# Kernel optimization log

Hardware: AMD Instinct MI355X
Metric: run time of the kernel (lower is better)

Reference implementation:

```python
import jax, jax.numpy as jnp
import numpy as np

D_MODEL = 1024
N_HEADS = 16
D_FF = 4096
B, T = 4, 2048
EPS = 1e-5


def layernorm(x, g, b):
    mu = jnp.mean(x, axis=-1, keepdims=True)
    var = jnp.var(x, axis=-1, keepdims=True)
    return (x - mu) * jax.lax.rsqrt(var + EPS) * g + b


def setup_inputs() -> dict:
    key = jax.random.key(0)
    ks = jax.random.split(key, 8)
    s = 0.02
    return {
        "x": jax.random.normal(ks[0], (B, T, D_MODEL), jnp.float32),
        "ln1_g": jnp.ones((D_MODEL,), jnp.float32),
        "ln1_b": jnp.zeros((D_MODEL,), jnp.float32),
        "wq": jax.random.normal(ks[1], (D_MODEL, D_MODEL), jnp.float32) * s,
        "bq": jnp.zeros((D_MODEL,), jnp.float32),
        "wk": jax.random.normal(ks[2], (D_MODEL, D_MODEL), jnp.float32) * s,
        "bk": jnp.zeros((D_MODEL,), jnp.float32),
        "wv": jax.random.normal(ks[3], (D_MODEL, D_MODEL), jnp.float32) * s,
        "bv": jnp.zeros((D_MODEL,), jnp.float32),
        "wo": jax.random.normal(ks[4], (D_MODEL, D_MODEL), jnp.float32) * s,
        "bo": jnp.zeros((D_MODEL,), jnp.float32),
        "ln2_g": jnp.ones((D_MODEL,), jnp.float32),
        "ln2_b": jnp.zeros((D_MODEL,), jnp.float32),
        "w1": jax.random.normal(ks[5], (D_FF, D_MODEL), jnp.float32) * s,
        "b1": jnp.zeros((D_FF,), jnp.float32),
        "w2": jax.random.normal(ks[6], (D_MODEL, D_FF), jnp.float32) * s,
        "b2": jnp.zeros((D_MODEL,), jnp.float32),
    }


def reference(x, ln1_g, ln1_b, wq, bq, wk, bk, wv, bv, wo, bo,
              ln2_g, ln2_b, w1, b1, w2, b2):
    d_k = D_MODEL // N_HEADS
    # --- attention sublayer (pre-LN) ---
    h = layernorm(x, ln1_g, ln1_b)                       # [B,T,D]
    q = (h @ wq.T + bq).reshape(B, T, N_HEADS, d_k)
    k = (h @ wk.T + bk).reshape(B, T, N_HEADS, d_k)
    v = (h @ wv.T + bv).reshape(B, T, N_HEADS, d_k)
    scores = jnp.einsum("bqhd,bkhd->bhqk", q, k) / jnp.sqrt(jnp.float32(d_k))
    attn = jax.nn.softmax(scores, axis=-1)               # [B,H,T,T]
    o = jnp.einsum("bhqk,bkhd->bqhd", attn, v).reshape(B, T, D_MODEL)
    x = x + (o @ wo.T + bo)
    # --- FFN sublayer ---
    h2 = layernorm(x, ln2_g, ln2_b)
    h2 = jax.nn.gelu(h2 @ w1.T + b1, approximate=False)  # torch GELU = exact erf
    x = x + (h2 @ w2.T + b2)
    return x
```

## Files before the change

kernel.cpp:

```cpp
#include <hip/hip_runtime.h>
#include <math.h>


#define D_MODEL 1024
#define D_FF    4096
#define NH      16
#define BATCH   4
#define SEQ     2048
#define DK      64
#define MTOK    (BATCH*SEQ)
#define NBH     (BATCH*NH)

typedef __bf16 bf16;
typedef _Float16 f16;
typedef bf16  bf16x4 __attribute__((ext_vector_type(4)));
typedef bf16  bf16x8 __attribute__((ext_vector_type(8)));
typedef f16   f16x4  __attribute__((ext_vector_type(4)));
typedef __fp16 hf16x2 __attribute__((ext_vector_type(2)));
typedef __fp16 hf16x4 __attribute__((ext_vector_type(4)));
typedef float f32x4  __attribute__((ext_vector_type(4)));

__device__ __forceinline__ void gload_lds16(const void* g, void* l) {
  __builtin_amdgcn_global_load_lds(
      (__attribute__((address_space(1))) void*)g,
      (__attribute__((address_space(3))) void*)l, 16, 0, 0);
}

#define BAR() __builtin_amdgcn_s_barrier()
#define WAIT_VM0() do { asm volatile("s_waitcnt vmcnt(0)" ::: "memory"); \
  __builtin_amdgcn_sched_barrier(0); } while (0)
#define WAIT_LGKM0() do { asm volatile("s_waitcnt lgkmcnt(0)" ::: "memory"); } while (0)

__global__ __launch_bounds__(256) void cast_w(const float* __restrict__ s,
                                              bf16* __restrict__ d, int n) {
  int i = (blockIdx.x * 256 + threadIdx.x) * 4;
  if (i >= n) return;
  float4 v = *(const float4*)(s + i);
  bf16x4 o;
  o[0] = (bf16)v.x; o[1] = (bf16)v.y; o[2] = (bf16)v.z; o[3] = (bf16)v.w;
  *(bf16x4*)(d + i) = o;
}

__global__ __launch_bounds__(256) void ln_kernel(const float* __restrict__ x,
                                                 const float* __restrict__ g,
                                                 const float* __restrict__ b,
                                                 bf16* __restrict__ out) {
  int row = blockIdx.x;
  int tid = threadIdx.x;
  const float* xr = x + (size_t)row * D_MODEL;
  float4 v = *(const float4*)(xr + tid * 4);
  float s  = v.x + v.y + v.z + v.w;
  float sq = v.x*v.x + v.y*v.y + v.z*v.z + v.w*v.w;
  #pragma unroll
  for (int off = 1; off < 64; off <<= 1) {
    s  += __shfl_xor(s,  off, 64);
    sq += __shfl_xor(sq, off, 64);
  }
  __shared__ float ls[4], lq[4];
  int wid = tid >> 6, lane = tid & 63;
  if (lane == 0) { ls[wid] = s; lq[wid] = sq; }
  __syncthreads();
  s  = ls[0] + ls[1] + ls[2] + ls[3];
  sq = lq[0] + lq[1] + lq[2] + lq[3];
  float mu   = s * (1.0f / D_MODEL);
  float var  = sq * (1.0f / D_MODEL) - mu * mu;
  float rstd = rsqrtf(var + 1e-5f);
  float4 gv = *(const float4*)(g + tid * 4);
  float4 bv = *(const float4*)(b + tid * 4);
  bf16x4 o;
  o[0] = (bf16)((v.x - mu) * rstd * gv.x + bv.x);
  o[1] = (bf16)((v.y - mu) * rstd * gv.y + bv.y);
  o[2] = (bf16)((v.z - mu) * rstd * gv.z + bv.z);
  o[3] = (bf16)((v.w - mu) * rstd * gv.w + bv.w);
  *(bf16x4*)(out + (size_t)row * D_MODEL + tid * 4) = o;
}

enum { EP_QKV = 0, EP_RESID = 1, EP_GELU = 2 };

#define QSCALE 0.18033688011112042f

template <int EP, int CFG>
__global__ __launch_bounds__(512) void gemm8p(
    const bf16* __restrict__ A, const bf16* __restrict__ W,
    const float* __restrict__ bias,
    const float* __restrict__ resid,
    float* __restrict__ out_f32,
    bf16* __restrict__ out_bf,
    int M, int N, int K) {
  constexpr int BM  = CFG ? 128 : 256;
  constexpr int BK  = CFG ? 64 : 32;
  constexpr int WM  = CFG ? 64 : 128;
  constexpr int FRN = WM / 16;
  constexpr int FRP = FRN / 2;
  constexpr int KKN = BK / 32;
  constexpr int RB  = BK * 2;
  constexpr int GR  = RB / 16;
  constexpr int RSH = CFG ? 7 : 6;
  constexpr int AB  = 16384;
  constexpr int TB  = AB + 256 * BK * 2;
  constexpr int L   = TB / 8192;
  constexpr int Lh  = L / 2;

  __shared__ char lds[3 * TB];

  int tiles_n = N >> 8;
  int nwg = (M / BM) * tiles_n;
  int bid = blockIdx.x;
  int swz = (bid & 7) * (nwg >> 3) + (bid >> 3);
  int bm = swz / tiles_n, bn = swz % tiles_n;
  int m0 = bm * BM, n0 = bn << 8;
  int tid = threadIdx.x, wid = tid >> 6, lane = tid & 63;
  int wm = wid >> 2, wn = wid & 3;
  int l15 = lane & 15, l4 = lane >> 4;

  f32x4 acc[FRN][4];
  #pragma unroll
  for (int i = 0; i < FRN; i++)
    #pragma unroll
    for (int j = 0; j < 4; j++)
      #pragma unroll
      for (int e = 0; e < 4; e++) acc[i][j][e] = 0.f;

  auto STAGE = [&](int kt, int nb, int part) {
    char* buf = lds + nb * TB;
    #pragma unroll
    for (int l = part * Lh; l < part * Lh + Lh; ++l) {
      bool isA = l < 2;
      int o = (isA ? l : l - 2) * 8192 + tid * 16;
      int row = o >> RSH;
      int g = (o >> 4) & (GR - 1);
      int gs = g ^ (CFG ? (row & 7) : ((row >> 1) & 3));
      const bf16* src = (isA ? A + (size_t)(m0 + row) * K
                             : W + (size_t)(n0 + row) * K) + kt * BK + gs * 8;
      gload_lds16(src, buf + (isA ? 0 : AB) + o);
    }
  };

  int nt = K / BK;
  STAGE(0, 0, 0); STAGE(0, 0, 1);
  STAGE(1, 1, 0); STAGE(1, 1, 1);
  if constexpr (CFG) { asm volatile("s_waitcnt vmcnt(6)" ::: "memory"); }
  else               { asm volatile("s_waitcnt vmcnt(4)" ::: "memory"); }
  __builtin_amdgcn_sched_barrier(0);
  BAR();

  bf16x8 bfr[4][KKN];
  for (int t = 0; t < nt; ++t) {
    int cb = t % 3, nb = cb >= 1 ? cb - 1 : 2;
    bool ds_ = (t + 2) < nt;
    const char* bc = lds + cb * TB;

    bf16x8 af[FRP][KKN];
    #pragma unroll
    for (int f = 0; f < FRP; ++f)
      #pragma unroll
      for (int kk = 0; kk < KKN; ++kk) {
        int row = wm * WM + f * 16 + l15;
        int g = (kk * 4 + l4) ^ (CFG ? (row & 7) : ((row >> 1) & 3));
        af[f][kk] = *(const bf16x8*)(bc + row * RB + g * 16);
      }
    #pragma unroll
    for (int fc = 0; fc < 4; ++fc)
      #pragma unroll
      for (int kk = 0; kk < KKN; ++kk) {
        int row = wn * 64 + fc * 16 + l15;
        int g = (kk * 4 + l4) ^ (CFG ? (row & 7) : ((row >> 1) & 3));
        bfr[fc][kk] = *(const bf16x8*)(bc + AB + row * RB + g * 16);
      }
    if (ds_) STAGE(t + 2, nb, 0);
    BAR();
    WAIT_LGKM0();
    __builtin_amdgcn_s_setprio(1);
    #pragma unroll
    for (int f = 0; f < FRP; ++f)
      #pragma unroll
      for (int fc = 0; fc < 4; ++fc)
        #pragma unroll
        for (int kk = 0; kk < KKN; ++kk)
          acc[f][fc] = __builtin_amdgcn_mfma_f32_16x16x32_bf16(af[f][kk], bfr[fc][kk],
                                                               acc[f][fc], 0, 0, 0);
    __builtin_amdgcn_s_setprio(0);
    BAR();

    bf16x8 af1[FRP][KKN];
    #pragma unroll
    for (int f = 0; f < FRP; ++f)
      #pragma unroll
      for (int kk = 0; kk < KKN; ++kk) {
        int row = wm * WM + (FRP + f) * 16 + l15;
        int g = (kk * 4 + l4) ^ (CFG ? (row & 7) : ((row >> 1) & 3));
        af1[f][kk] = *(const bf16x8*)(bc + row * RB + g * 16);
      }
    if (ds_) STAGE(t + 2, nb, 1);
    BAR();
    WAIT_LGKM0();
    __builtin_amdgcn_s_setprio(1);
    #pragma unroll
    for (int f = 0; f < FRP; ++f)
      #pragma unroll
      for (int fc = 0; fc < 4; ++fc)
        #pragma unroll
        for (int kk = 0; kk < KKN; ++kk)
          acc[FRP + f][fc] = __builtin_amdgcn_mfma_f32_16x16x32_bf16(af1[f][kk], bfr[fc][kk],
                                                                     acc[FRP + f][fc], 0, 0, 0);
    __builtin_amdgcn_s_setprio(0);
    if (t < nt - 2) {
      if constexpr (CFG) { asm volatile("s_waitcnt vmcnt(6)" ::: "memory"); }
      else               { asm volatile("s_waitcnt vmcnt(4)" ::: "memory"); }
      __builtin_amdgcn_sched_barrier(0);
    } else if (t == nt - 2) {
      WAIT_VM0();
    }
    BAR();
  }

  if (EP == EP_QKV) {
    #pragma unroll
    for (int i = 0; i < FRN; i++)
      #pragma unroll
      for (int j = 0; j < 4; j++) {
        int gm0 = m0 + wm * WM + i * 16 + (l4 << 2);
        int gn  = n0 + wn * 64 + j * 16 + l15;
        int which = gn >> 10;
        int nn = gn & 1023, head = nn >> 6, d = nn & 63;
        int bb = gm0 >> 11, t = gm0 & 2047;
        float bv = bias[gn];
        if (which == 2) {
          f16x4 pk;
          #pragma unroll
          for (int jj = 0; jj < 4; jj++) pk[jj] = (f16)(acc[i][j][jj] + bv);
          *(f16x4*)((f16*)out_bf + (size_t)2 * NBH * SEQ * DK +
                    ((size_t)(bb * NH + head) * DK + d) * SEQ + t) = pk;
        } else {
          float scale = (which == 0) ? QSCALE : 1.0f;
          #pragma unroll
          for (int jj = 0; jj < 4; jj++) {
            float cv = (acc[i][j][jj] + bv) * scale;
            size_t idx = (size_t)which * (NBH * SEQ * DK) +
                         ((size_t)(bb * NH + head) * SEQ + (t + jj)) * DK + d;
            out_bf[idx] = (bf16)cv;
          }
        }
      }
  } else {
    #pragma unroll
    for (int i = 0; i < FRN; i++)
      #pragma unroll
      for (int j = 0; j < 4; j++)
        #pragma unroll
        for (int jj = 0; jj < 4; jj++) {
          int gm = m0 + wm * WM + i * 16 + (l4 << 2) + jj;
          int gn = n0 + wn * 64 + j * 16 + l15;
          float cv = acc[i][j][jj] + bias[gn];
          if (EP == EP_RESID) {
            size_t idx = (size_t)gm * N + gn;
            out_f32[idx] = resid[idx] + cv;
          } else {
            float ge = 0.5f * cv * (1.0f + erff(cv * 0.70710678118654752f));
            out_bf[(size_t)gm * N + gn] = (bf16)ge;
          }
        }
  }
}

__global__ __launch_bounds__(256) void attn_kernel(
    const bf16* __restrict__ q, const bf16* __restrict__ k,
    const f16* __restrict__ vt, bf16* __restrict__ o) {
  __shared__ bf16 kt_lds[2][128 * 64];
  __shared__ f16  vt_lds[2][64 * 128];
  int bid = blockIdx.x;
  int bh = bid >> 5;
  int qt = bid & 31;
  int t0 = qt << 6;
  int tid = threadIdx.x, wid = tid >> 6, lane = tid & 63;
  int l15 = lane & 15, l4 = lane >> 4;

  int kb0 = l15 * 128 + ((l4 ^ (l15 & 7)) << 4);
  int kb1 = l15 * 128 + (((4 + l4) ^ (l15 & 7)) << 4);
  int vb[8];
  #pragma unroll
  for (int kk = 0; kk < 8; kk++)
    vb[kk] = l15 * 256 + (((((kk << 1) + (l4 >> 1)) ^ l15) << 4) + ((l4 & 1) << 3));

  const bf16* qbase = q + ((size_t)bh * SEQ + t0 + wid * 16 + l15) * DK;
  bf16x8 qf[2];
  qf[0] = *(const bf16x8*)(qbase + (l4 << 3));
  qf[1] = *(const bf16x8*)(qbase + 32 + (l4 << 3));

  const f16x4 vones = {(f16)1.f, (f16)1.f, (f16)1.f, (f16)1.f};
  float m_run = -1e30f;
  f32x4 acc_o[4];
  f32x4 acc_l;
  #pragma unroll
  for (int nd = 0; nd < 4; nd++)
    #pragma unroll
    for (int e = 0; e < 4; e++) acc_o[nd][e] = 0.f;
  #pragma unroll
  for (int e = 0; e < 4; e++) acc_l[e] = 0.f;

  int rK = tid >> 3;
  int cK = ((tid & 7) ^ (rK & 7)) << 3;
  const bf16* gK = k + ((size_t)bh * SEQ + rK) * DK + cK;
  int rV = tid >> 4;
  int cV = ((tid & 15) ^ rV) << 3;
  const f16* gV = vt + ((size_t)bh * DK + rV) * SEQ + cV;

  auto stage = [&](int buf, int t) {
    const bf16* gKt = gK + ((size_t)t * 128) * DK;
    const f16*  gVt = gV + t * 128;
    char* dK = (char*)&kt_lds[buf][0] + (wid << 10);
    char* dV = (char*)&vt_lds[buf][0] + (wid << 10);
    #pragma unroll
    for (int it = 0; it < 4; ++it) {
      gload_lds16(gKt + (size_t)(it * 32) * DK, dK + it * 4096);
      gload_lds16(gVt + (size_t)(it * 16) * SEQ, dV + it * 4096);
    }
  };

  stage(0, 0);
  WAIT_VM0();
  BAR();

  for (int t = 0; t < SEQ / 128; ++t) {
    int cur = t & 1;
    if (t < SEQ / 128 - 1) stage(cur ^ 1, t + 1);
    const char* kbase = (const char*)&kt_lds[cur][0];
    const char* vbase = (const char*)&vt_lds[cur][0];

    f32x4 accs[8];
    #pragma unroll
    for (int n = 0; n < 8; n++)
      #pragma unroll
      for (int e = 0; e < 4; e++) accs[n][e] = 0.f;
    __builtin_amdgcn_s_setprio(1);
    #pragma unroll
    for (int n = 0; n < 8; n++) {
      bf16x8 kf0 = *(const bf16x8*)(kbase + kb0 + n * 2048);
      bf16x8 kf1 = *(const bf16x8*)(kbase + kb1 + n * 2048);
      accs[n] = __builtin_amdgcn_mfma_f32_16x16x32_bf16(kf0, qf[0], accs[n], 0, 0, 0);
      accs[n] = __builtin_amdgcn_mfma_f32_16x16x32_bf16(kf1, qf[1], accs[n], 0, 0, 0);
    }
    __builtin_amdgcn_s_setprio(0);

    float mloc = -1e30f;
    #pragma unroll
    for (int n = 0; n < 8; n++) {
      float a0 = fmaxf(accs[n][0], accs[n][1]);
      float a1 = fmaxf(accs[n][2], accs[n][3]);
      mloc = fmaxf(mloc, fmaxf(a0, a1));
    }
    float mt = fmaxf(mloc, __shfl_xor(mloc, 16, 64));
    mt = fmaxf(mt, __shfl_xor(mt, 32, 64));
    if (__any(mt > m_run + 8.0f)) {
      float mn = fmaxf(m_run, mt);
      float sc = __builtin_amdgcn_exp2f(m_run - mn);
      m_run = mn;
      float scr0 = __shfl(sc, l4 * 20 + 0, 64);
      float scr1 = __shfl(sc, l4 * 20 + 1, 64);
      float scr2 = __shfl(sc, l4 * 20 + 2, 64);
      float scr3 = __shfl(sc, l4 * 20 + 3, 64);
      #pragma unroll
      for (int nd = 0; nd < 4; nd++) {
        acc_o[nd][0] *= scr0; acc_o[nd][1] *= scr1;
        acc_o[nd][2] *= scr2; acc_o[nd][3] *= scr3;
      }
      acc_l[0] *= scr0; acc_l[1] *= scr1; acc_l[2] *= scr2; acc_l[3] *= scr3;
    }
    f16x4 pa[8];
    #pragma unroll
    for (int n = 0; n < 8; n++) {
      float e0 = __builtin_amdgcn_exp2f(accs[n][0] - m_run);
      float e1 = __builtin_amdgcn_exp2f(accs[n][1] - m_run);
      float e2 = __builtin_amdgcn_exp2f(accs[n][2] - m_run);
      float e3 = __builtin_amdgcn_exp2f(accs[n][3] - m_run);
      hf16x2 lo = __builtin_amdgcn_cvt_pkrtz(e0, e1);
      hf16x2 hi = __builtin_amdgcn_cvt_pkrtz(e2, e3);
      hf16x4 cmb = __builtin_shufflevector(lo, hi, 0, 1, 2, 3);
      pa[n] = __builtin_bit_cast(f16x4, cmb);
    }

    __builtin_amdgcn_s_setprio(1);
    #pragma unroll
    for (int kk = 0; kk < 8; kk++) {
      #pragma unroll
      for (int nd = 0; nd < 4; nd++) {
        f16x4 vf = *(const f16x4*)(vbase + vb[kk] + nd * 4096);
        acc_o[nd] = __builtin_amdgcn_mfma_f32_16x16x16f16(pa[kk], vf, acc_o[nd], 0, 0, 0);
      }
      acc_l = __builtin_amdgcn_mfma_f32_16x16x16f16(pa[kk], vones, acc_l, 0, 0, 0);
    }
    __builtin_amdgcn_s_setprio(0);

    if (t < SEQ / 128 - 1) { WAIT_VM0(); }
    BAR();
  }

  float rl0 = 1.0f / acc_l[0], rl1 = 1.0f / acc_l[1];
  float rl2 = 1.0f / acc_l[2], rl3 = 1.0f / acc_l[3];
  int bb = bh >> 4, hh = bh & 15;
  #pragma unroll
  for (int nd = 0; nd < 4; nd++) {
    int d = nd * 16 + l15;
    int rowb = t0 + wid * 16 + l4 * 4;
    o[((size_t)bb * SEQ + rowb + 0) * D_MODEL + hh * DK + d] = (bf16)(acc_o[nd][0] * rl0);
    o[((size_t)bb * SEQ + rowb + 1) * D_MODEL + hh * DK + d] = (bf16)(acc_o[nd][1] * rl1);
    o[((size_t)bb * SEQ + rowb + 2) * D_MODEL + hh * DK + d] = (bf16)(acc_o[nd][2] * rl2);
    o[((size_t)bb * SEQ + rowb + 3) * D_MODEL + hh * DK + d] = (bf16)(acc_o[nd][3] * rl3);
  }
}

extern "C" void kernel_launch(void* const* d_in, const int* in_sizes, int n_in,
                              void* d_out, int out_size, void* d_ws, size_t ws_size,
                              hipStream_t stream) {
  const float* x    = (const float*)d_in[0];
  const float* ln1g = (const float*)d_in[1];
  const float* ln1b = (const float*)d_in[2];
  const float* wq   = (const float*)d_in[3];
  const float* bq   = (const float*)d_in[4];
  const float* wk   = (const float*)d_in[5];
  const float* bk   = (const float*)d_in[6];
  const float* wv   = (const float*)d_in[7];
  const float* bv   = (const float*)d_in[8];
  const float* wo   = (const float*)d_in[9];
  const float* bo   = (const float*)d_in[10];
  const float* ln2g = (const float*)d_in[11];
  const float* ln2b = (const float*)d_in[12];
  const float* w1   = (const float*)d_in[13];
  const float* b1   = (const float*)d_in[14];
  const float* w2   = (const float*)d_in[15];
  const float* b2   = (const float*)d_in[16];
  float* out = (float*)d_out;

  char* ws = (char*)d_ws;
  bf16* wqkv_b = (bf16*)(ws);
  bf16* wo_b   = (bf16*)(ws + ((size_t)6  << 20));
  bf16* w1_b   = (bf16*)(ws + ((size_t)8  << 20));
  bf16* w2_b   = (bf16*)(ws + ((size_t)16 << 20));
  bf16* h_b    = (bf16*)(ws + ((size_t)24 << 20));
  bf16* qkv_b  = (bf16*)(ws + ((size_t)40 << 20));
  bf16* o_b    = (bf16*)(ws + ((size_t)88 << 20));
  bf16* ffn1_b = (bf16*)(ws + ((size_t)40 << 20));
  float* bqkv  = (float*)(ws + ((size_t)104 << 20));

  cast_w<<<1024, 256, 0, stream>>>(wq, wqkv_b, 1 << 20);
  cast_w<<<1024, 256, 0, stream>>>(wk, wqkv_b + (1 << 20), 1 << 20);
  cast_w<<<1024, 256, 0, stream>>>(wv, wqkv_b + (2 << 20), 1 << 20);
  cast_w<<<1024, 256, 0, stream>>>(wo, wo_b, 1 << 20);
  cast_w<<<4096, 256, 0, stream>>>(w1, w1_b, 1 << 22);
  cast_w<<<4096, 256, 0, stream>>>(w2, w2_b, 1 << 22);
  (void)hipMemcpyAsync(bqkv,        bq, 4096, hipMemcpyDeviceToDevice, stream);
  (void)hipMemcpyAsync(bqkv + 1024, bk, 4096, hipMemcpyDeviceToDevice, stream);
  (void)hipMemcpyAsync(bqkv + 2048, bv, 4096, hipMemcpyDeviceToDevice, stream);

  ln_kernel<<<MTOK, 256, 0, stream>>>(x, ln1g, ln1b, h_b);
  gemm8p<EP_QKV, 1><<<768, 512, 0, stream>>>(h_b, wqkv_b, bqkv, nullptr, nullptr,
                                             qkv_b, MTOK, 3072, 1024);
  attn_kernel<<<NBH * 32, 256, 0, stream>>>(qkv_b, qkv_b + (size_t)NBH * SEQ * DK,
                                            (const f16*)(qkv_b + (size_t)2 * NBH * SEQ * DK),
                                            o_b);
  gemm8p<EP_RESID, 1><<<256, 512, 0, stream>>>(o_b, wo_b, bo, x, out, nullptr,
                                               MTOK, 1024, 1024);
  ln_kernel<<<MTOK, 256, 0, stream>>>(out, ln2g, ln2b, h_b);
  gemm8p<EP_GELU, 0><<<512, 512, 0, stream>>>(h_b, w1_b, b1, nullptr, nullptr,
                                              ffn1_b, MTOK, 4096, 1024);
  gemm8p<EP_RESID, 1><<<256, 512, 0, stream>>>(ffn1_b, w2_b, b2, out, out, nullptr,
                                               MTOK, 1024, 4096);
}
```

Measured before the change: 476.7 us.

## Split-K the FFN2 GEMM with fp16 partials, retile QKV, relayout attention V LDS

The FFN2 GEMM is split into two K halves. Each half runs as a 256-row-tile block and writes fp16 partial sums, and a new combine kernel adds the residual, the bias and both partials. The QKV projection switches to the larger 256-row tile config with fewer blocks. The attention kernel's V tile in LDS is reorganised into two 64-key halves with a new XOR swizzle and new staging addresses, presumably to cut LDS bank conflicts. The trade-offs are extra global traffic for the partials plus an extra launch, and lower precision because the partials are stored as fp16.

```diff
diff --git a/kernel.cpp b/kernel.cpp
--- a/kernel.cpp
+++ b/kernel.cpp
@@ -75,7 +75,25 @@
   *(bf16x4*)(out + (size_t)row * D_MODEL + tid * 4) = o;
 }
 
-enum { EP_QKV = 0, EP_RESID = 1, EP_GELU = 2 };
+__global__ __launch_bounds__(256) void ffn2_combine(const float* __restrict__ x,
+                                                    const float* __restrict__ b2,
+                                                    const f16* __restrict__ p0,
+                                                    const f16* __restrict__ p1,
+                                                    float* __restrict__ out) {
+  size_t i = ((size_t)blockIdx.x * 256 + threadIdx.x) * 4;
+  float4 xv = *(const float4*)(x + i);
+  f16x4 a = *(const f16x4*)(p0 + i);
+  f16x4 c = *(const f16x4*)(p1 + i);
+  float4 bv = *(const float4*)(b2 + (i & 1023));
+  float4 o;
+  o.x = xv.x + bv.x + (float)a[0] + (float)c[0];
+  o.y = xv.y + bv.y + (float)a[1] + (float)c[1];
+  o.z = xv.z + bv.z + (float)a[2] + (float)c[2];
+  o.w = xv.w + bv.w + (float)a[3] + (float)c[3];
+  *(float4*)(out + i) = o;
+}
+
+enum { EP_QKV = 0, EP_RESID = 1, EP_GELU = 2, EP_PART = 3 };
 
 #define QSCALE 0.18033688011112042f
 
@@ -86,7 +104,7 @@
     const float* __restrict__ resid,
     float* __restrict__ out_f32,
     bf16* __restrict__ out_bf,
-    int M, int N, int K) {
+    int M, int N, int K, int lda) {
   constexpr int BM  = CFG ? 128 : 256;
   constexpr int BK  = CFG ? 64 : 32;
   constexpr int WM  = CFG ? 64 : 128;
@@ -106,6 +124,8 @@
   int tiles_n = N >> 8;
   int nwg = (M / BM) * tiles_n;
   int bid = blockIdx.x;
+  int kh = 0;
+  if (EP == EP_PART) { if (bid >= nwg) { kh = 1; bid -= nwg; } }
   int swz = (bid & 7) * (nwg >> 3) + (bid >> 3);
   int bm = swz / tiles_n, bn = swz % tiles_n;
   int m0 = bm * BM, n0 = bn << 8;
@@ -113,6 +133,9 @@
   int wm = wid >> 2, wn = wid & 3;
   int l15 = lane & 15, l4 = lane >> 4;
 
+  const bf16* Ap = A + (size_t)kh * K;
+  const bf16* Wp = W + (size_t)kh * K;
+
   f32x4 acc[FRN][4];
   #pragma unroll
   for (int i = 0; i < FRN; i++)
@@ -130,8 +153,8 @@
       int row = o >> RSH;
       int g = (o >> 4) & (GR - 1);
       int gs = g ^ (CFG ? (row & 7) : ((row >> 1) & 3));
-      const bf16* src = (isA ? A + (size_t)(m0 + row) * K
-                             : W + (size_t)(n0 + row) * K) + kt * BK + gs * 8;
+      const bf16* src = (isA ? Ap + (size_t)(m0 + row) * lda
+                             : Wp + (size_t)(n0 + row) * lda) + kt * BK + gs * 8;
       gload_lds16(src, buf + (isA ? 0 : AB) + o);
     }
   };
@@ -242,6 +265,18 @@
           }
         }
       }
+  } else if (EP == EP_PART) {
+    f16* dst = kh ? (f16*)out_bf : (f16*)out_f32;
+    #pragma unroll
+    for (int i = 0; i < FRN; i++)
+      #pragma unroll
+      for (int j = 0; j < 4; j++)
+        #pragma unroll
+        for (int jj = 0; jj < 4; jj++) {
+          int gm = m0 + wm * WM + i * 16 + (l4 << 2) + jj;
+          int gn = n0 + wn * 64 + j * 16 + l15;
+          dst[(size_t)gm * N + gn] = (f16)acc[i][j][jj];
+        }
   } else {
     #pragma unroll
     for (int i = 0; i < FRN; i++)
@@ -267,7 +302,7 @@
     const bf16* __restrict__ q, const bf16* __restrict__ k,
     const f16* __restrict__ vt, bf16* __restrict__ o) {
   __shared__ bf16 kt_lds[2][128 * 64];
-  __shared__ f16  vt_lds[2][64 * 128];
+  __shared__ f16  vt_lds[2][128 * 64];
   int bid = blockIdx.x;
   int bh = bid >> 5;
   int qt = bid & 31;
@@ -280,7 +315,8 @@
   int vb[8];
   #pragma unroll
   for (int kk = 0; kk < 8; kk++)
-    vb[kk] = l15 * 256 + (((((kk << 1) + (l4 >> 1)) ^ l15) << 4) + ((l4 & 1) << 3));
+    vb[kk] = ((kk >> 2) << 13) + l15 * 128 +
+             (((((kk & 3) << 1) + (l4 >> 1)) ^ (l15 & 7)) << 4) + ((l4 & 1) << 3);
 
   const bf16* qbase = q + ((size_t)bh * SEQ + t0 + wid * 16 + l15) * DK;
   bf16x8 qf[2];
@@ -301,19 +337,24 @@
   int rK = tid >> 3;
   int cK = ((tid & 7) ^ (rK & 7)) << 3;
   const bf16* gK = k + ((size_t)bh * SEQ + rK) * DK + cK;
-  int rV = tid >> 4;
-  int cV = ((tid & 15) ^ rV) << 3;
-  const f16* gV = vt + ((size_t)bh * DK + rV) * SEQ + cV;
+  const f16* gVsrc[4];
+  #pragma unroll
+  for (int it = 0; it < 4; ++it) {
+    int R = it * 32 + wid * 8 + (lane >> 3);
+    int g = lane & 7;
+    gVsrc[it] = vt + (size_t)bh * DK * SEQ + (size_t)(R & 63) * SEQ +
+                ((R >> 6) << 6) + ((g ^ (R & 7)) << 3);
+  }
 
   auto stage = [&](int buf, int t) {
     const bf16* gKt = gK + ((size_t)t * 128) * DK;
-    const f16*  gVt = gV + t * 128;
+    int kv0 = t * 128;
     char* dK = (char*)&kt_lds[buf][0] + (wid << 10);
     char* dV = (char*)&vt_lds[buf][0] + (wid << 10);
     #pragma unroll
     for (int it = 0; it < 4; ++it) {
       gload_lds16(gKt + (size_t)(it * 32) * DK, dK + it * 4096);
-      gload_lds16(gVt + (size_t)(it * 16) * SEQ, dV + it * 4096);
+      gload_lds16(gVsrc[it] + kv0, dV + it * 4096);
     }
   };
 
@@ -384,7 +425,7 @@
     for (int kk = 0; kk < 8; kk++) {
       #pragma unroll
       for (int nd = 0; nd < 4; nd++) {
-        f16x4 vf = *(const f16x4*)(vbase + vb[kk] + nd * 4096);
+        f16x4 vf = *(const f16x4*)(vbase + vb[kk] + nd * 2048);
         acc_o[nd] = __builtin_amdgcn_mfma_f32_16x16x16f16(pa[kk], vf, acc_o[nd], 0, 0, 0);
       }
       acc_l = __builtin_amdgcn_mfma_f32_16x16x16f16(pa[kk], vones, acc_l, 0, 0, 0);
@@ -441,6 +482,8 @@
   bf16* o_b    = (bf16*)(ws + ((size_t)88 << 20));
   bf16* ffn1_b = (bf16*)(ws + ((size_t)40 << 20));
   float* bqkv  = (float*)(ws + ((size_t)104 << 20));
+  f16* p0      = (f16*)(ws);
+  f16* p1      = (f16*)(ws + ((size_t)24 << 20));
 
   cast_w<<<1024, 256, 0, stream>>>(wq, wqkv_b, 1 << 20);
   cast_w<<<1024, 256, 0, stream>>>(wk, wqkv_b + (1 << 20), 1 << 20);
@@ -453,16 +496,18 @@
   (void)hipMemcpyAsync(bqkv + 2048, bv, 4096, hipMemcpyDeviceToDevice, stream);
 
   ln_kernel<<<MTOK, 256, 0, stream>>>(x, ln1g, ln1b, h_b);
-  gemm8p<EP_QKV, 1><<<768, 512, 0, stream>>>(h_b, wqkv_b, bqkv, nullptr, nullptr,
-                                             qkv_b, MTOK, 3072, 1024);
+  gemm8p<EP_QKV, 0><<<384, 512, 0, stream>>>(h_b, wqkv_b, bqkv, nullptr, nullptr,
+                                             qkv_b, MTOK, 3072, 1024, 1024);
   attn_kernel<<<NBH * 32, 256, 0, stream>>>(qkv_b, qkv_b + (size_t)NBH * SEQ * DK,
                                             (const f16*)(qkv_b + (size_t)2 * NBH * SEQ * DK),
                                             o_b);
   gemm8p<EP_RESID, 1><<<256, 512, 0, stream>>>(o_b, wo_b, bo, x, out, nullptr,
-                                               MTOK, 1024, 1024);
+                                               MTOK, 1024, 1024, 1024);
   ln_kernel<<<MTOK, 256, 0, stream>>>(out, ln2g, ln2b, h_b);
   gemm8p<EP_GELU, 0><<<512, 512, 0, stream>>>(h_b, w1_b, b1, nullptr, nullptr,
-                                              ffn1_b, MTOK, 4096, 1024);
-  gemm8p<EP_RESID, 1><<<256, 512, 0, stream>>>(ffn1_b, w2_b, b2, out, out, nullptr,
-                                               MTOK, 1024, 4096);
-}
+                                              ffn1_b, MTOK, 4096, 1024, 1024);
+  gemm8p<EP_PART, 0><<<256, 512, 0, stream>>>(ffn1_b, w2_b, nullptr, nullptr,
+                                              (float*)p0, (bf16*)p1,
+                                              MTOK, 1024, 2048, 4096);
+  ffn2_combine<<<8192, 256, 0, stream>>>(out, b2, p0, p1, out);
+}
```

After: 485.9 us. About the same (+1.9%).

## Use 16x16x32 f16 MFMA for attention PV with permuted V layout

Applied to the files above, without the earlier changes.

Switches the attention P·V product from 16x16x16 f16 MFMAs to the wider 16x16x32 f16 MFMA, packing eight softmax probabilities per operand. To make this work, the QKV epilogue writes V-transposed with a permuted sequence order, and the LDS staging addresses and swizzle for V are reworked so each lane reads 8 contiguous f16 values with one 16-byte LDS load. The goal is half as many MFMA issues and LDS reads in the PV loop, at the cost of a tightly coupled permutation between the QKV writer and the attention reader that must stay consistent.

```diff
diff --git a/kernel.cpp b/kernel.cpp
--- a/kernel.cpp
+++ b/kernel.cpp
@@ -16,8 +16,10 @@
 typedef bf16  bf16x4 __attribute__((ext_vector_type(4)));
 typedef bf16  bf16x8 __attribute__((ext_vector_type(8)));
 typedef f16   f16x4  __attribute__((ext_vector_type(4)));
+typedef f16   f16x8  __attribute__((ext_vector_type(8)));
 typedef __fp16 hf16x2 __attribute__((ext_vector_type(2)));
 typedef __fp16 hf16x4 __attribute__((ext_vector_type(4)));
+typedef __fp16 hf16x8 __attribute__((ext_vector_type(8)));
 typedef float f32x4  __attribute__((ext_vector_type(4)));
 
 __device__ __forceinline__ void gload_lds16(const void* g, void* l) {
@@ -226,11 +228,12 @@
         int bb = gm0 >> 11, t = gm0 & 2047;
         float bv = bias[gn];
         if (which == 2) {
+          int sbase = (t & ~31) + ((t >> 2) & 3) * 8 + ((t >> 4) & 1) * 4;
           f16x4 pk;
           #pragma unroll
           for (int jj = 0; jj < 4; jj++) pk[jj] = (f16)(acc[i][j][jj] + bv);
           *(f16x4*)((f16*)out_bf + (size_t)2 * NBH * SEQ * DK +
-                    ((size_t)(bb * NH + head) * DK + d) * SEQ + t) = pk;
+                    ((size_t)(bb * NH + head) * DK + d) * SEQ + sbase) = pk;
         } else {
           float scale = (which == 0) ? QSCALE : 1.0f;
           #pragma unroll
@@ -277,17 +280,19 @@
 
   int kb0 = l15 * 128 + ((l4 ^ (l15 & 7)) << 4);
   int kb1 = l15 * 128 + (((4 + l4) ^ (l15 & 7)) << 4);
-  int vb[8];
-  #pragma unroll
-  for (int kk = 0; kk < 8; kk++)
-    vb[kk] = l15 * 256 + (((((kk << 1) + (l4 >> 1)) ^ l15) << 4) + ((l4 & 1) << 3));
+  int vb32[4];
+  #pragma unroll
+  for (int n = 0; n < 4; n++)
+    vb32[n] = l15 * 256 + (((n * 4 + l4) ^ (l15 & 7)) << 4);
 
   const bf16* qbase = q + ((size_t)bh * SEQ + t0 + wid * 16 + l15) * DK;
   bf16x8 qf[2];
   qf[0] = *(const bf16x8*)(qbase + (l4 << 3));
   qf[1] = *(const bf16x8*)(qbase + 32 + (l4 << 3));
 
-  const f16x4 vones = {(f16)1.f, (f16)1.f, (f16)1.f, (f16)1.f};
+  f16x8 vones8;
+  #pragma unroll
+  for (int e = 0; e < 8; e++) vones8[e] = (f16)1.f;
   float m_run = -1e30f;
   f32x4 acc_o[4];
   f32x4 acc_l;
@@ -301,19 +306,25 @@
   int rK = tid >> 3;
   int cK = ((tid & 7) ^ (rK & 7)) << 3;
   const bf16* gK = k + ((size_t)bh * SEQ + rK) * DK + cK;
-  int rV = tid >> 4;
-  int cV = ((tid & 15) ^ rV) << 3;
-  const f16* gV = vt + ((size_t)bh * DK + rV) * SEQ + cV;
+  const f16* gVsrc[4];
+  #pragma unroll
+  for (int it = 0; it < 4; ++it) {
+    int ob = it * 4096 + tid * 16;
+    int d  = ob >> 8;
+    int gd = (ob >> 4) & 15;
+    gVsrc[it] = vt + (size_t)bh * DK * SEQ + (size_t)d * SEQ +
+                ((gd ^ (d & 7)) << 3);
+  }
 
   auto stage = [&](int buf, int t) {
     const bf16* gKt = gK + ((size_t)t * 128) * DK;
-    const f16*  gVt = gV + t * 128;
+    int kv0 = t * 128;
     char* dK = (char*)&kt_lds[buf][0] + (wid << 10);
     char* dV = (char*)&vt_lds[buf][0] + (wid << 10);
     #pragma unroll
     for (int it = 0; it < 4; ++it) {
       gload_lds16(gKt + (size_t)(it * 32) * DK, dK + it * 4096);
-      gload_lds16(gVt + (size_t)(it * 16) * SEQ, dV + it * 4096);
+      gload_lds16(gVsrc[it] + kv0, dV + it * 4096);
     }
   };
 
@@ -366,28 +377,36 @@
       }
       acc_l[0] *= scr0; acc_l[1] *= scr1; acc_l[2] *= scr2; acc_l[3] *= scr3;
     }
-    f16x4 pa[8];
-    #pragma unroll
-    for (int n = 0; n < 8; n++) {
-      float e0 = __builtin_amdgcn_exp2f(accs[n][0] - m_run);
-      float e1 = __builtin_amdgcn_exp2f(accs[n][1] - m_run);
-      float e2 = __builtin_amdgcn_exp2f(accs[n][2] - m_run);
-      float e3 = __builtin_amdgcn_exp2f(accs[n][3] - m_run);
-      hf16x2 lo = __builtin_amdgcn_cvt_pkrtz(e0, e1);
-      hf16x2 hi = __builtin_amdgcn_cvt_pkrtz(e2, e3);
-      hf16x4 cmb = __builtin_shufflevector(lo, hi, 0, 1, 2, 3);
-      pa[n] = __builtin_bit_cast(f16x4, cmb);
+    f16x8 pa32[4];
+    #pragma unroll
+    for (int n = 0; n < 4; n++) {
+      float e0 = __builtin_amdgcn_exp2f(accs[2*n][0] - m_run);
+      float e1 = __builtin_amdgcn_exp2f(accs[2*n][1] - m_run);
+      float e2 = __builtin_amdgcn_exp2f(accs[2*n][2] - m_run);
+      float e3 = __builtin_amdgcn_exp2f(accs[2*n][3] - m_run);
+      float e4 = __builtin_amdgcn_exp2f(accs[2*n+1][0] - m_run);
+      float e5 = __builtin_amdgcn_exp2f(accs[2*n+1][1] - m_run);
+      float e6 = __builtin_amdgcn_exp2f(accs[2*n+1][2] - m_run);
+      float e7 = __builtin_amdgcn_exp2f(accs[2*n+1][3] - m_run);
+      hf16x2 p01 = __builtin_amdgcn_cvt_pkrtz(e0, e1);
+      hf16x2 p23 = __builtin_amdgcn_cvt_pkrtz(e2, e3);
+      hf16x2 p45 = __builtin_amdgcn_cvt_pkrtz(e4, e5);
+      hf16x2 p67 = __builtin_amdgcn_cvt_pkrtz(e6, e7);
+      hf16x4 lo = __builtin_shufflevector(p01, p23, 0, 1, 2, 3);
+      hf16x4 hi = __builtin_shufflevector(p45, p67, 0, 1, 2, 3);
+      hf16x8 cmb = __builtin_shufflevector(lo, hi, 0, 1, 2, 3, 4, 5, 6, 7);
+      pa32[n] = __builtin_bit_cast(f16x8, cmb);
     }
 
     __builtin_amdgcn_s_setprio(1);
     #pragma unroll
-    for (int kk = 0; kk < 8; kk++) {
+    for (int n = 0; n < 4; n++) {
       #pragma unroll
       for (int nd = 0; nd < 4; nd++) {
-        f16x4 vf = *(const f16x4*)(vbase + vb[kk] + nd * 4096);
-        acc_o[nd] = __builtin_amdgcn_mfma_f32_16x16x16f16(pa[kk], vf, acc_o[nd], 0, 0, 0);
-      }
-      acc_l = __builtin_amdgcn_mfma_f32_16x16x16f16(pa[kk], vones, acc_l, 0, 0, 0);
+        f16x8 vf = *(const f16x8*)(vbase + vb32[n] + nd * 4096);
+        acc_o[nd] = __builtin_amdgcn_mfma_f32_16x16x32_f16(pa32[n], vf, acc_o[nd], 0, 0, 0);
+      }
+      acc_l = __builtin_amdgcn_mfma_f32_16x16x32_f16(pa32[n], vones8, acc_l, 0, 0, 0);
     }
     __builtin_amdgcn_s_setprio(0);
 
```

Result: faster. 453.5 us (-4.9%).
